# Performance work log

Hardware: AMD Instinct MI355X
Metric: run time of the kernel (lower is better)

## Reference

```python
import jax, jax.numpy as jnp
import numpy as np

N_NODES = 50000
N_EDGES = 600000
F_IN, HID, N_CLS = 128, 128, 40
NEG_SLOPE = 0.2


def _gat_conv(x, src, dst, W, a_src, a_dst, b, num_nodes):
    # x: [N, Fin] -> h: [N, H]  (heads=1 PyG GATConv)
    h = x @ W
    s_src = h @ a_src  # [N]
    s_dst = h @ a_dst  # [N]
    e = jax.nn.leaky_relu(s_src[src] + s_dst[dst], NEG_SLOPE)  # [E]
    # numerically-stable softmax over incoming edges per destination node
    m = jax.ops.segment_max(e, dst, num_segments=num_nodes)  # [N]
    ex = jnp.exp(e - m[dst])
    denom = jax.ops.segment_sum(ex, dst, num_segments=num_nodes)  # [N]
    alpha = ex / denom[dst]  # [E]
    out = jax.ops.segment_sum(alpha[:, None] * h[src], dst, num_segments=num_nodes)
    return out + b


def setup_inputs() -> dict:
    key = jax.random.key(0)
    ks = jax.random.split(key, 10)
    x = jax.random.normal(ks[0], (N_NODES, F_IN), dtype=jnp.float32)
    edge_index = jax.random.randint(ks[1], (2, N_EDGES), 0, N_NODES, dtype=jnp.int64)
    sd = lambda fin: 1.0 / np.sqrt(fin)
    return {
        "x": x,
        "edge_index": edge_index,
        "W1": jax.random.normal(ks[2], (F_IN, HID), dtype=jnp.float32) * sd(F_IN),
        "a1_src": jax.random.normal(ks[3], (HID,), dtype=jnp.float32) * sd(HID),
        "a1_dst": jax.random.normal(ks[4], (HID,), dtype=jnp.float32) * sd(HID),
        "b1": jnp.zeros((HID,), dtype=jnp.float32),
        "W2": jax.random.normal(ks[5], (HID, HID), dtype=jnp.float32) * sd(HID),
        "a2_src": jax.random.normal(ks[6], (HID,), dtype=jnp.float32) * sd(HID),
        "a2_dst": jax.random.normal(ks[7], (HID,), dtype=jnp.float32) * sd(HID),
        "b2": jnp.zeros((HID,), dtype=jnp.float32),
        "Wl": jax.random.normal(ks[8], (HID, N_CLS), dtype=jnp.float32) * sd(HID),
        "bl": jnp.zeros((N_CLS,), dtype=jnp.float32),
    }


def reference(x, edge_index, W1, a1_src, a1_dst, b1, W2, a2_src, a2_dst, b2, Wl, bl):
    n = x.shape[0]
    # PyG GATConv adds self loops by default
    loops = jnp.arange(n, dtype=edge_index.dtype)
    src = jnp.concatenate([edge_index[0], loops])
    dst = jnp.concatenate([edge_index[1], loops])
    h = jax.nn.relu(_gat_conv(x, src, dst, W1, a1_src, a1_dst, b1, n))
    # F.dropout(training=self.training): eval mode -> identity
    h = _gat_conv(h, src, dst, W2, a2_src, a2_dst, b2, n)
    logits = jax.nn.log_softmax(h @ Wl + bl, axis=1)
    return (logits, edge_index)
```

## Files before the change

kernel.cpp:

```cpp
#include <hip/hip_runtime.h>
#include <hip/hip_bf16.h>
#include <math.h>

#define N_NODES 50000
#define N_EDGES 600000
#define TOT_E   (N_EDGES + N_NODES)
#define FDIM    128
#define HROW    64
#define NCLS    40
#define SCAN_B  1024

typedef __attribute__((ext_vector_type(4))) float  f32x4;
typedef __attribute__((ext_vector_type(8))) __bf16 bf16x8;
union FragU { uint32_t u[4]; bf16x8 v; };

__device__ inline float bf16_lo(uint32_t u) { return __uint_as_float(u << 16); }
__device__ inline float bf16_hi(uint32_t u) { return __uint_as_float(u & 0xffff0000u); }
__device__ inline uint32_t bf16_pack(float a, float b) {
    uint32_t ua = __float_as_uint(a), ub = __float_as_uint(b);
    uint32_t ra = (ua + 0x7fffu + ((ua >> 16) & 1u)) >> 16;
    uint32_t rb = (ub + 0x7fffu + ((ub >> 16) & 1u)) >> 16;
    return ra | (rb << 16);
}

__device__ __forceinline__ void wave_agg_loop(
        const uint4* __restrict__ h4, const float* __restrict__ ssrc,
        const int* __restrict__ adj, float sd, int beg, int deg,
        float* wb, int* sb, int lane, int sub, int l16,
        float acc[8], float& dsum) {
    for (int base = 0; base < deg; base += 64) {
        int c = min(64, deg - base);
        int s = 0; float w = 0.f;
        if (lane < c) {
            s = adj[beg + base + lane];
            float e = ssrc[s] + sd;
            e = (e >= 0.f) ? e : 0.2f * e;
            w = __expf(e);
        }
        wb[lane] = w;
        sb[lane] = s;
        dsum += w;
        asm volatile("s_waitcnt lgkmcnt(0)" ::: "memory");

        int rounds = (c + 15) >> 4;
        for (int t = 0; t < rounds; t++) {
            int j = t * 16 + 4 * sub;
            float4 w4 = *(const float4*)&wb[j];
            int4   s4 = *(const int4*)&sb[j];
            uint4 u0 = h4[(size_t)s4.x * 16 + l16];
            uint4 u1 = h4[(size_t)s4.y * 16 + l16];
            uint4 u2 = h4[(size_t)s4.z * 16 + l16];
            uint4 u3 = h4[(size_t)s4.w * 16 + l16];
            acc[0] += w4.x * bf16_lo(u0.x) + w4.y * bf16_lo(u1.x) + w4.z * bf16_lo(u2.x) + w4.w * bf16_lo(u3.x);
            acc[1] += w4.x * bf16_hi(u0.x) + w4.y * bf16_hi(u1.x) + w4.z * bf16_hi(u2.x) + w4.w * bf16_hi(u3.x);
            acc[2] += w4.x * bf16_lo(u0.y) + w4.y * bf16_lo(u1.y) + w4.z * bf16_lo(u2.y) + w4.w * bf16_lo(u3.y);
            acc[3] += w4.x * bf16_hi(u0.y) + w4.y * bf16_hi(u1.y) + w4.z * bf16_hi(u2.y) + w4.w * bf16_hi(u3.y);
            acc[4] += w4.x * bf16_lo(u0.z) + w4.y * bf16_lo(u1.z) + w4.z * bf16_lo(u2.z) + w4.w * bf16_lo(u3.z);
            acc[5] += w4.x * bf16_hi(u0.z) + w4.y * bf16_hi(u1.z) + w4.z * bf16_hi(u2.z) + w4.w * bf16_hi(u3.z);
            acc[6] += w4.x * bf16_lo(u0.w) + w4.y * bf16_lo(u1.w) + w4.z * bf16_lo(u2.w) + w4.w * bf16_lo(u3.w);
            acc[7] += w4.x * bf16_hi(u0.w) + w4.y * bf16_hi(u1.w) + w4.z * bf16_hi(u2.w) + w4.w * bf16_hi(u3.w);
        }
        asm volatile("" ::: "memory");
    }
    #pragma unroll
    for (int k = 0; k < 8; k++) {
        acc[k] += __shfl_xor(acc[k], 16, 64);
        acc[k] += __shfl_xor(acc[k], 32, 64);
    }
    #pragma unroll
    for (int off = 32; off > 0; off >>= 1) dsum += __shfl_xor(dsum, off, 64);
}

#define PACK_BLOCKS  12500
#define WFRAG_BLOCKS 16
#define HIST_BLOCKS  ((N_EDGES / 4 + 255) / 256)
__global__ __launch_bounds__(256) void k1_setup_hist(
        const float* __restrict__ x, uint32_t* __restrict__ Xp,
        const float* __restrict__ W1, const float* __restrict__ W2,
        uint32_t* __restrict__ wf1, uint32_t* __restrict__ wf2,
        const int* __restrict__ ei, int* __restrict__ counts) {
    int b = blockIdx.x;
    if (b < PACK_BLOCKS) {
        int i = b * 256 + threadIdx.x;
        float2 v = ((const float2*)x)[i];
        Xp[i] = bf16_pack(v.x, v.y);
        return;
    }
    if (b < PACK_BLOCKS + WFRAG_BLOCKS) {
        int t = (b - PACK_BLOCKS) * 256 + threadIdx.x;
        if (t >= 4096) return;
        const float* W = (t < 2048) ? W1 : W2;
        uint32_t*   wf = (t < 2048) ? wf1 : wf2;
        int q = t & 2047;
        int lane = q & 63, nt = (q >> 6) & 7, kt = q >> 9;
        int n = nt * 16 + (lane & 15), g = lane >> 4;
        uint32_t frag[4];
        #pragma unroll
        for (int d = 0; d < 4; d++) {
            int kb = kt * 32 + 4 * g + (d & 1) * 2 + (d >> 1) * 16;
            frag[d] = bf16_pack(W[kb * FDIM + n], W[(kb + 1) * FDIM + n]);
        }
        ((uint4*)wf)[(kt * 8 + nt) * 64 + lane] = *(uint4*)frag;
        return;
    }
    int i = (b - PACK_BLOCKS - WFRAG_BLOCKS) * 256 + threadIdx.x;
    if (i >= N_EDGES / 4) return;
    int4 d = ((const int4*)(ei + N_EDGES))[i];
    atomicAdd(&counts[d.x], 1);
    atomicAdd(&counts[d.y], 1);
    atomicAdd(&counts[d.z], 1);
    atomicAdd(&counts[d.w], 1);
}

__global__ void scan1_kernel(const int* __restrict__ counts, int* __restrict__ excl,
                             int* __restrict__ bsums, int n) {
    __shared__ int ws[16];
    int gid = blockIdx.x * SCAN_B + threadIdx.x;
    int wv = threadIdx.x >> 6, lane = threadIdx.x & 63;
    int v = (gid < n) ? (counts[gid] + 1) : 0;
    int incl = v;
    #pragma unroll
    for (int off = 1; off < 64; off <<= 1) {
        int t = __shfl_up(incl, off, 64);
        if (lane >= off) incl += t;
    }
    if (lane == 63) ws[wv] = incl;
    __syncthreads();
    int woff = 0;
    for (int i = 0; i < wv; i++) woff += ws[i];
    if (gid < n) excl[gid] = woff + incl - v;
    if (threadIdx.x == SCAN_B - 1) bsums[blockIdx.x] = woff + incl;
}

__global__ void scan3_kernel(int* __restrict__ rowptr, const int* __restrict__ bsums,
                             int* __restrict__ cursor, int n, int total) {
    __shared__ int base_s;
    if (threadIdx.x < 64) {
        int v = (threadIdx.x < (int)blockIdx.x) ? bsums[threadIdx.x] : 0;
        #pragma unroll
        for (int off = 32; off > 0; off >>= 1) v += __shfl_down(v, off, 64);
        if (threadIdx.x == 0) base_s = v;
    }
    __syncthreads();
    int base = base_s;
    int gid = blockIdx.x * SCAN_B + threadIdx.x;
    if (gid < n) {
        int v = rowptr[gid] + base;
        rowptr[gid] = v;
        cursor[gid] = v;
    }
    if (gid == 0) rowptr[n] = total;
}

#define SCAT_T      ((N_EDGES / 4) + N_NODES)
#define SCAT_BLOCKS ((SCAT_T + 255) / 256)
#define GEMM_BLOCKS ((N_NODES + 63) / 64)
#define EDGE_ITEMS  ((2 * N_EDGES) / 4)
#define EDGE_BLOCKS ((EDGE_ITEMS + 255) / 256)
__global__ __launch_bounds__(256) void k4_scatter_gemm_edge(
        const int* __restrict__ ei, int* __restrict__ cursor, int* __restrict__ adj,
        const uint32_t* __restrict__ Xp, const uint32_t* __restrict__ wf,
        const float* __restrict__ a_s, const float* __restrict__ a_d,
        uint32_t* __restrict__ H, float* __restrict__ ssrc, float* __restrict__ sdst,
        float* __restrict__ eout) {
    int b = blockIdx.x;
    if (b < SCAT_BLOCKS) {
        int i = b * 256 + threadIdx.x;
        if (i >= SCAT_T) return;
        if (i < N_EDGES / 4) {
            int4 s4 = ((const int4*)ei)[i];
            int4 d4 = ((const int4*)(ei + N_EDGES))[i];
            adj[atomicAdd(&cursor[d4.x], 1)] = s4.x;
            adj[atomicAdd(&cursor[d4.y], 1)] = s4.y;
            adj[atomicAdd(&cursor[d4.z], 1)] = s4.z;
            adj[atomicAdd(&cursor[d4.w], 1)] = s4.w;
        } else {
            int nd = i - N_EDGES / 4;
            adj[atomicAdd(&cursor[nd], 1)] = nd;
        }
        return;
    }
    if (b < SCAT_BLOCKS + GEMM_BLOCKS) {
        int lane = threadIdx.x & 63, wv = threadIdx.x >> 6;
        int row0 = (b - SCAT_BLOCKS) * 64 + wv * 16;
        if (row0 >= N_NODES) return;
        int r = lane & 15, g = lane >> 4;

        const uint32_t* xrow = Xp + (size_t)(row0 + r) * HROW + 2 * g;
        FragU af[4];
        #pragma unroll
        for (int kt = 0; kt < 4; kt++) {
            uint2 lo = *(const uint2*)(xrow + kt * 16);
            uint2 hi = *(const uint2*)(xrow + kt * 16 + 8);
            af[kt].u[0] = lo.x; af[kt].u[1] = lo.y;
            af[kt].u[2] = hi.x; af[kt].u[3] = hi.y;
        }
        f32x4 acc[8] = {};
        #pragma unroll
        for (int kt = 0; kt < 4; kt++) {
            #pragma unroll
            for (int nt = 0; nt < 8; nt++) {
                FragU bfr;
                *(uint4*)bfr.u = ((const uint4*)wf)[(kt * 8 + nt) * 64 + lane];
                acc[nt] = __builtin_amdgcn_mfma_f32_16x16x32_bf16(af[kt].v, bfr.v, acc[nt], 0, 0, 0);
            }
        }
        float av_s[8], av_d[8];
        #pragma unroll
        for (int nt = 0; nt < 8; nt++) { av_s[nt] = a_s[16 * nt + r]; av_d[nt] = a_d[16 * nt + r]; }
        #pragma unroll
        for (int j = 0; j < 4; j++) {
            float ps = 0.f, pd = 0.f;
            #pragma unroll
            for (int nt = 0; nt < 8; nt++) { ps += acc[nt][j] * av_s[nt]; pd += acc[nt][j] * av_d[nt]; }
            #pragma unroll
            for (int off = 1; off < 16; off <<= 1) {
                ps += __shfl_xor(ps, off, 64);
                pd += __shfl_xor(pd, off, 64);
            }
            if (r == 0) { ssrc[row0 + 4 * g + j] = ps; sdst[row0 + 4 * g + j] = pd; }
        }
        #pragma unroll
        for (int nt = 0; nt < 8; nt++) {
            #pragma unroll
            for (int j = 0; j < 4; j++) {
                float v0 = acc[nt][j];
                float v1 = __shfl_xor(v0, 1, 64);
                if (!(r & 1))
                    H[(size_t)(row0 + 4 * g + j) * HROW + nt * 8 + (r >> 1)] = bf16_pack(v0, v1);
            }
        }
        return;
    }
    int i = (b - SCAT_BLOCKS - GEMM_BLOCKS) * 256 + threadIdx.x;
    if (i < EDGE_ITEMS) {
        int4 v = ((const int4*)ei)[i];
        ((float4*)eout)[i] = make_float4((float)v.x, (float)v.y, (float)v.z, (float)v.w);
    }
}

__global__ __launch_bounds__(256) void k5_agg_gemm(
        const uint32_t* __restrict__ h, const float* __restrict__ ssrc,
        const float* __restrict__ sdst, const int* __restrict__ rowptr,
        const int* __restrict__ adj, const float* __restrict__ bias,
        const uint32_t* __restrict__ wf, const float* __restrict__ a_s,
        const float* __restrict__ a_d, uint32_t* __restrict__ Hout,
        float* __restrict__ ssrc2, float* __restrict__ sdst2) {
    int tid = threadIdx.x;
    int wv = tid >> 6, lane = tid & 63;
    int sub = lane >> 4, l16 = lane & 15;
    int row0 = blockIdx.x * 16;
    __shared__ __align__(16) float    wbuf[4][64];
    __shared__ __align__(16) int      sbuf[4][64];
    __shared__ __align__(16) uint32_t rowbuf[16][68];
    __shared__ float scS[4][16], scD[4][16];
    const uint4* h4 = (const uint4*)h;

    for (int i = 0; i < 4; i++) {
        int row = wv * 4 + i;
        int n = row0 + row;
        int beg = rowptr[n], deg = rowptr[n + 1] - beg;
        float acc[8] = {};
        float dsum = 0.f;
        wave_agg_loop(h4, ssrc, adj, sdst[n], beg, deg, wbuf[wv], sbuf[wv],
                      lane, sub, l16, acc, dsum);
        if (sub == 0) {
            float inv = 1.f / dsum;
            float4 b0 = *(const float4*)&bias[l16 * 8];
            float4 b1 = *(const float4*)&bias[l16 * 8 + 4];
            float v0 = fmaxf(acc[0] * inv + b0.x, 0.f), v1 = fmaxf(acc[1] * inv + b0.y, 0.f);
            float v2 = fmaxf(acc[2] * inv + b0.z, 0.f), v3 = fmaxf(acc[3] * inv + b0.w, 0.f);
            float v4 = fmaxf(acc[4] * inv + b1.x, 0.f), v5 = fmaxf(acc[5] * inv + b1.y, 0.f);
            float v6 = fmaxf(acc[6] * inv + b1.z, 0.f), v7 = fmaxf(acc[7] * inv + b1.w, 0.f);
            uint4 o;
            o.x = bf16_pack(v0, v1); o.y = bf16_pack(v2, v3);
            o.z = bf16_pack(v4, v5); o.w = bf16_pack(v6, v7);
            *(uint4*)&rowbuf[row][l16 * 4] = o;
        }
    }
    __syncthreads();

    int r = lane & 15, g = lane >> 4;
    FragU af[4];
    #pragma unroll
    for (int kt = 0; kt < 4; kt++) {
        uint2 lo = *(const uint2*)&rowbuf[r][kt * 16 + 2 * g];
        uint2 hi = *(const uint2*)&rowbuf[r][kt * 16 + 2 * g + 8];
        af[kt].u[0] = lo.x; af[kt].u[1] = lo.y;
        af[kt].u[2] = hi.x; af[kt].u[3] = hi.y;
    }
    f32x4 acc2[2] = {};
    #pragma unroll
    for (int kt = 0; kt < 4; kt++) {
        #pragma unroll
        for (int t = 0; t < 2; t++) {
            int nt = 2 * wv + t;
            FragU bfr;
            *(uint4*)bfr.u = ((const uint4*)wf)[(kt * 8 + nt) * 64 + lane];
            acc2[t] = __builtin_amdgcn_mfma_f32_16x16x32_bf16(af[kt].v, bfr.v, acc2[t], 0, 0, 0);
        }
    }
    float as0 = a_s[16 * (2 * wv) + r], as1 = a_s[16 * (2 * wv + 1) + r];
    float ad0 = a_d[16 * (2 * wv) + r], ad1 = a_d[16 * (2 * wv + 1) + r];
    #pragma unroll
    for (int j = 0; j < 4; j++) {
        float ps = acc2[0][j] * as0 + acc2[1][j] * as1;
        float pd = acc2[0][j] * ad0 + acc2[1][j] * ad1;
        #pragma unroll
        for (int off = 1; off < 16; off <<= 1) {
            ps += __shfl_xor(ps, off, 64);
            pd += __shfl_xor(pd, off, 64);
        }
        if (r == 0) { scS[wv][4 * g + j] = ps; scD[wv][4 * g + j] = pd; }
    }
    #pragma unroll
    for (int t = 0; t < 2; t++) {
        #pragma unroll
        for (int j = 0; j < 4; j++) {
            float v0 = acc2[t][j];
            float v1 = __shfl_xor(v0, 1, 64);
            if (!(r & 1))
                Hout[(size_t)(row0 + 4 * g + j) * HROW + (2 * wv + t) * 8 + (r >> 1)] = bf16_pack(v0, v1);
        }
    }
    __syncthreads();
    if (tid < 16)
        ssrc2[row0 + tid] = scS[0][tid] + scS[1][tid] + scS[2][tid] + scS[3][tid];
    else if (tid < 32) {
        int q = tid - 16;
        sdst2[row0 + q] = scD[0][q] + scD[1][q] + scD[2][q] + scD[3][q];
    }
}

__global__ __launch_bounds__(256) void k6_agg_cls(
        const uint32_t* __restrict__ h, const float* __restrict__ ssrc,
        const float* __restrict__ sdst, const int* __restrict__ rowptr,
        const int* __restrict__ adj, const float* __restrict__ bias,
        const float* __restrict__ Wl, const float* __restrict__ bl,
        float* __restrict__ out) {
    int tid = threadIdx.x;
    int wv = tid >> 6, lane = tid & 63;
    int sub = lane >> 4, l16 = lane & 15;
    int row0 = blockIdx.x * 16;
    __shared__ __align__(16) float wbuf[4][64];
    __shared__ __align__(16) int   sbuf[4][64];
    __shared__ float xs[16][FDIM];
    const uint4* h4 = (const uint4*)h;

    for (int i = 0; i < 4; i++) {
        int row = wv * 4 + i;
        int n = row0 + row;
        int beg = rowptr[n], deg = rowptr[n + 1] - beg;
        float acc[8] = {};
        float dsum = 0.f;
        wave_agg_loop(h4, ssrc, adj, sdst[n], beg, deg, wbuf[wv], sbuf[wv],
                      lane, sub, l16, acc, dsum);
        if (sub == 0) {
            float inv = 1.f / dsum;
            float4 b0 = *(const float4*)&bias[l16 * 8];
            float4 b1 = *(const float4*)&bias[l16 * 8 + 4];
            float4 p0, p1;
            p0.x = acc[0] * inv + b0.x; p0.y = acc[1] * inv + b0.y;
            p0.z = acc[2] * inv + b0.z; p0.w = acc[3] * inv + b0.w;
            p1.x = acc[4] * inv + b1.x; p1.y = acc[5] * inv + b1.y;
            p1.z = acc[6] * inv + b1.z; p1.w = acc[7] * inv + b1.w;
            *(float4*)&xs[row][l16 * 8]     = p0;
            *(float4*)&xs[row][l16 * 8 + 4] = p1;
        }
    }
    __syncthreads();

    int c = tid & 63, hw = tid >> 6;
    float acc[4];
    float blc = (c < NCLS) ? bl[c] : 0.f;
    #pragma unroll
    for (int r = 0; r < 4; r++) acc[r] = blc;

    #pragma unroll 2
    for (int k = 0; k < FDIM; k += 4) {
        float w0 = 0.f, w1 = 0.f, w2 = 0.f, w3 = 0.f;
        if (c < NCLS) {
            w0 = Wl[(k + 0) * NCLS + c]; w1 = Wl[(k + 1) * NCLS + c];
            w2 = Wl[(k + 2) * NCLS + c]; w3 = Wl[(k + 3) * NCLS + c];
        }
        #pragma unroll
        for (int r = 0; r < 4; r++) {
            float4 xv = *(const float4*)&xs[hw * 4 + r][k];
            acc[r] += xv.x * w0 + xv.y * w1 + xv.z * w2 + xv.w * w3;
        }
    }
    #pragma unroll
    for (int r = 0; r < 4; r++) {
        float v = (c < NCLS) ? acc[r] : -INFINITY;
        float mx = v;
        #pragma unroll
        for (int off = 32; off > 0; off >>= 1) mx = fmaxf(mx, __shfl_xor(mx, off, 64));
        float ex = (c < NCLS) ? expf(v - mx) : 0.f;
        #pragma unroll
        for (int off = 32; off > 0; off >>= 1) ex += __shfl_xor(ex, off, 64);
        float ls = logf(ex);
        if (c < NCLS) out[(size_t)(row0 + hw * 4 + r) * NCLS + c] = v - mx - ls;
    }
}

extern "C" void kernel_launch(void* const* d_in, const int* in_sizes, int n_in,
                              void* d_out, int out_size, void* d_ws, size_t ws_size,
                              hipStream_t stream) {
    const float* x   = (const float*)d_in[0];
    const int*   ei  = (const int*)d_in[1];
    const float* W1  = (const float*)d_in[2];
    const float* a1s = (const float*)d_in[3];
    const float* a1d = (const float*)d_in[4];
    const float* b1  = (const float*)d_in[5];
    const float* W2  = (const float*)d_in[6];
    const float* a2s = (const float*)d_in[7];
    const float* a2d = (const float*)d_in[8];
    const float* b2  = (const float*)d_in[9];
    const float* Wl  = (const float*)d_in[10];
    const float* bl  = (const float*)d_in[11];
    float* out = (float*)d_out;

    char* ws = (char*)d_ws;
    size_t off = 0;
    auto alloc = [&](size_t bytes) {
        void* p = ws + off;
        off = (off + bytes + 255) & ~(size_t)255;
        return p;
    };
    int*      row_ptr = (int*)alloc((N_NODES + 1) * sizeof(int));
    int*      cursor  = (int*)alloc(N_NODES * sizeof(int));
    int*      counts  = (int*)alloc(N_NODES * sizeof(int));
    int*      bsums   = (int*)alloc(64 * sizeof(int));
    int*      adj     = (int*)alloc(TOT_E * sizeof(int));
    uint32_t* Xp      = (uint32_t*)alloc((size_t)N_NODES * HROW * sizeof(uint32_t));
    uint32_t* hA      = (uint32_t*)alloc((size_t)N_NODES * HROW * sizeof(uint32_t));
    uint32_t* hB      = (uint32_t*)alloc((size_t)N_NODES * HROW * sizeof(uint32_t));
    float*    ssrc    = (float*)alloc(N_NODES * sizeof(float));
    float*    sdst    = (float*)alloc(N_NODES * sizeof(float));
    float*    ssrc2   = (float*)alloc(N_NODES * sizeof(float));
    float*    sdst2   = (float*)alloc(N_NODES * sizeof(float));
    uint32_t* wf1     = (uint32_t*)alloc(2048 * 4 * sizeof(uint32_t));
    uint32_t* wf2     = (uint32_t*)alloc(2048 * 4 * sizeof(uint32_t));

    hipMemsetAsync(counts, 0, N_NODES * sizeof(int), stream);

    hipLaunchKernelGGL(k1_setup_hist, dim3(PACK_BLOCKS + WFRAG_BLOCKS + HIST_BLOCKS), dim3(256),
                       0, stream, x, Xp, W1, W2, wf1, wf2, ei, counts);

    int nscan = (N_NODES + SCAN_B - 1) / SCAN_B;
    hipLaunchKernelGGL(scan1_kernel, dim3(nscan), dim3(SCAN_B), 0, stream, counts, row_ptr, bsums, N_NODES);
    hipLaunchKernelGGL(scan3_kernel, dim3(nscan), dim3(SCAN_B), 0, stream, row_ptr, bsums, cursor, N_NODES, TOT_E);

    hipLaunchKernelGGL(k4_scatter_gemm_edge, dim3(SCAT_BLOCKS + GEMM_BLOCKS + EDGE_BLOCKS), dim3(256),
                       0, stream, ei, cursor, adj, Xp, wf1, a1s, a1d, hA, ssrc, sdst,
                       out + (size_t)N_NODES * NCLS);

    hipLaunchKernelGGL(k5_agg_gemm, dim3(N_NODES / 16), dim3(256), 0, stream,
                       hA, ssrc, sdst, row_ptr, adj, b1, wf2, a2s, a2d, hB, ssrc2, sdst2);

    hipLaunchKernelGGL(k6_agg_cls, dim3(N_NODES / 16), dim3(256), 0, stream,
                       hB, ssrc2, sdst2, row_ptr, adj, b2, Wl, bl, out);
}
```

Measured before the change: 269.2 us.

## Pad CSR rows to multiples of 16 and compute attention weights block-wide

Rounds each node's adjacency segment up to a multiple of 16 entries, zero-filling the padded adjacency buffer, so the aggregation loop runs without tail handling and reads source indices straight from global memory. Edge attention weights for a block's 16 rows are computed cooperatively into shared memory before aggregation, replacing the per-wave 64-edge chunking. Blocks grow to 512 threads with two rows per wave, and the MFMA and classifier stages are re-split to match. The padding adds zero-index edges whose weight is masked to zero, and it enlarges the adjacency buffer and the zeroing work. Rows whose padded segment exceeds the 1024-entry shared buffer would overflow it.

```diff
diff --git a/kernel.cpp b/kernel.cpp
--- a/kernel.cpp
+++ b/kernel.cpp
@@ -4,11 +4,11 @@
 
 #define N_NODES 50000
 #define N_EDGES 600000
-#define TOT_E   (N_EDGES + N_NODES)
 #define FDIM    128
 #define HROW    64
 #define NCLS    40
 #define SCAN_B  1024
+#define PADMAX  1400000
 
 typedef __attribute__((ext_vector_type(4))) float  f32x4;
 typedef __attribute__((ext_vector_type(8))) __bf16 bf16x8;
@@ -23,62 +23,71 @@
     return ra | (rb << 16);
 }
 
-__device__ __forceinline__ void wave_agg_loop(
-        const uint4* __restrict__ h4, const float* __restrict__ ssrc,
-        const int* __restrict__ adj, float sd, int beg, int deg,
-        float* wb, int* sb, int lane, int sub, int l16,
-        float acc[8], float& dsum) {
-    for (int base = 0; base < deg; base += 64) {
-        int c = min(64, deg - base);
-        int s = 0; float w = 0.f;
-        if (lane < c) {
-            s = adj[beg + base + lane];
-            float e = ssrc[s] + sd;
+__device__ __forceinline__ void block_weights(
+        const int* __restrict__ adj, const float* __restrict__ ssrc,
+        const int* rowL, const int* rdegL, const float* sdL,
+        float* wlds, int tid) {
+    int beg0 = rowL[0], range = rowL[16] - beg0;
+    for (int i = tid; i < range; i += 512) {
+        int gi = beg0 + i;
+        int nn = 0;
+        if (gi >= rowL[nn + 8]) nn += 8;
+        if (gi >= rowL[nn + 4]) nn += 4;
+        if (gi >= rowL[nn + 2]) nn += 2;
+        if (gi >= rowL[nn + 1]) nn += 1;
+        float w = 0.f;
+        if (gi - rowL[nn] < rdegL[nn]) {
+            float e = ssrc[adj[gi]] + sdL[nn];
             e = (e >= 0.f) ? e : 0.2f * e;
             w = __expf(e);
         }
-        wb[lane] = w;
-        sb[lane] = s;
-        dsum += w;
-        asm volatile("s_waitcnt lgkmcnt(0)" ::: "memory");
-
-        int rounds = (c + 15) >> 4;
-        for (int t = 0; t < rounds; t++) {
-            int j = t * 16 + 4 * sub;
-            float4 w4 = *(const float4*)&wb[j];
-            int4   s4 = *(const int4*)&sb[j];
-            uint4 u0 = h4[(size_t)s4.x * 16 + l16];
-            uint4 u1 = h4[(size_t)s4.y * 16 + l16];
-            uint4 u2 = h4[(size_t)s4.z * 16 + l16];
-            uint4 u3 = h4[(size_t)s4.w * 16 + l16];
-            acc[0] += w4.x * bf16_lo(u0.x) + w4.y * bf16_lo(u1.x) + w4.z * bf16_lo(u2.x) + w4.w * bf16_lo(u3.x);
-            acc[1] += w4.x * bf16_hi(u0.x) + w4.y * bf16_hi(u1.x) + w4.z * bf16_hi(u2.x) + w4.w * bf16_hi(u3.x);
-            acc[2] += w4.x * bf16_lo(u0.y) + w4.y * bf16_lo(u1.y) + w4.z * bf16_lo(u2.y) + w4.w * bf16_lo(u3.y);
-            acc[3] += w4.x * bf16_hi(u0.y) + w4.y * bf16_hi(u1.y) + w4.z * bf16_hi(u2.y) + w4.w * bf16_hi(u3.y);
-            acc[4] += w4.x * bf16_lo(u0.z) + w4.y * bf16_lo(u1.z) + w4.z * bf16_lo(u2.z) + w4.w * bf16_lo(u3.z);
-            acc[5] += w4.x * bf16_hi(u0.z) + w4.y * bf16_hi(u1.z) + w4.z * bf16_hi(u2.z) + w4.w * bf16_hi(u3.z);
-            acc[6] += w4.x * bf16_lo(u0.w) + w4.y * bf16_lo(u1.w) + w4.z * bf16_lo(u2.w) + w4.w * bf16_lo(u3.w);
-            acc[7] += w4.x * bf16_hi(u0.w) + w4.y * bf16_hi(u1.w) + w4.z * bf16_hi(u2.w) + w4.w * bf16_hi(u3.w);
-        }
-        asm volatile("" ::: "memory");
+        wlds[i] = w;
+    }
+}
+
+__device__ __forceinline__ void wave_agg(
+        const uint4* __restrict__ h4, const int* __restrict__ adj,
+        const float* wlds, int beg0, int beg, int pdeg,
+        int sub, int l16, float acc[8], float& dsum) {
+    int rounds = pdeg >> 4;
+    for (int t = 0; t < rounds; t++) {
+        int j = beg + t * 16 + 4 * sub;
+        float4 w4 = *(const float4*)&wlds[j - beg0];
+        int4   s4 = *(const int4*)&adj[j];
+        uint4 u0 = h4[(size_t)s4.x * 16 + l16];
+        uint4 u1 = h4[(size_t)s4.y * 16 + l16];
+        uint4 u2 = h4[(size_t)s4.z * 16 + l16];
+        uint4 u3 = h4[(size_t)s4.w * 16 + l16];
+        dsum += (w4.x + w4.y) + (w4.z + w4.w);
+        acc[0] += w4.x * bf16_lo(u0.x) + w4.y * bf16_lo(u1.x) + w4.z * bf16_lo(u2.x) + w4.w * bf16_lo(u3.x);
+        acc[1] += w4.x * bf16_hi(u0.x) + w4.y * bf16_hi(u1.x) + w4.z * bf16_hi(u2.x) + w4.w * bf16_hi(u3.x);
+        acc[2] += w4.x * bf16_lo(u0.y) + w4.y * bf16_lo(u1.y) + w4.z * bf16_lo(u2.y) + w4.w * bf16_lo(u3.y);
+        acc[3] += w4.x * bf16_hi(u0.y) + w4.y * bf16_hi(u1.y) + w4.z * bf16_hi(u2.y) + w4.w * bf16_hi(u3.y);
+        acc[4] += w4.x * bf16_lo(u0.z) + w4.y * bf16_lo(u1.z) + w4.z * bf16_lo(u2.z) + w4.w * bf16_lo(u3.z);
+        acc[5] += w4.x * bf16_hi(u0.z) + w4.y * bf16_hi(u1.z) + w4.z * bf16_hi(u2.z) + w4.w * bf16_hi(u3.z);
+        acc[6] += w4.x * bf16_lo(u0.w) + w4.y * bf16_lo(u1.w) + w4.z * bf16_lo(u2.w) + w4.w * bf16_lo(u3.w);
+        acc[7] += w4.x * bf16_hi(u0.w) + w4.y * bf16_hi(u1.w) + w4.z * bf16_hi(u2.w) + w4.w * bf16_hi(u3.w);
     }
     #pragma unroll
     for (int k = 0; k < 8; k++) {
         acc[k] += __shfl_xor(acc[k], 16, 64);
         acc[k] += __shfl_xor(acc[k], 32, 64);
     }
-    #pragma unroll
-    for (int off = 32; off > 0; off >>= 1) dsum += __shfl_xor(dsum, off, 64);
+    dsum += __shfl_xor(dsum, 16, 64);
+    dsum += __shfl_xor(dsum, 32, 64);
 }
 
 #define PACK_BLOCKS  12500
 #define WFRAG_BLOCKS 16
 #define HIST_BLOCKS  ((N_EDGES / 4 + 255) / 256)
+#define ADJZ_ITEMS   (PADMAX / 4)
+#define ADJZ_BLOCKS  ((ADJZ_ITEMS + 255) / 256)
 __global__ __launch_bounds__(256) void k1_setup_hist(
         const float* __restrict__ x, uint32_t* __restrict__ Xp,
         const float* __restrict__ W1, const float* __restrict__ W2,
         uint32_t* __restrict__ wf1, uint32_t* __restrict__ wf2,
-        const int* __restrict__ ei, int* __restrict__ counts) {
+        const int* __restrict__ ei, int* __restrict__ counts,
+        int* __restrict__ adj) {
     int b = blockIdx.x;
     if (b < PACK_BLOCKS) {
         int i = b * 256 + threadIdx.x;
@@ -103,13 +112,18 @@
         ((uint4*)wf)[(kt * 8 + nt) * 64 + lane] = *(uint4*)frag;
         return;
     }
-    int i = (b - PACK_BLOCKS - WFRAG_BLOCKS) * 256 + threadIdx.x;
-    if (i >= N_EDGES / 4) return;
-    int4 d = ((const int4*)(ei + N_EDGES))[i];
-    atomicAdd(&counts[d.x], 1);
-    atomicAdd(&counts[d.y], 1);
-    atomicAdd(&counts[d.z], 1);
-    atomicAdd(&counts[d.w], 1);
+    if (b < PACK_BLOCKS + WFRAG_BLOCKS + HIST_BLOCKS) {
+        int i = (b - PACK_BLOCKS - WFRAG_BLOCKS) * 256 + threadIdx.x;
+        if (i >= N_EDGES / 4) return;
+        int4 d = ((const int4*)(ei + N_EDGES))[i];
+        atomicAdd(&counts[d.x], 1);
+        atomicAdd(&counts[d.y], 1);
+        atomicAdd(&counts[d.z], 1);
+        atomicAdd(&counts[d.w], 1);
+        return;
+    }
+    int i = (b - PACK_BLOCKS - WFRAG_BLOCKS - HIST_BLOCKS) * 256 + threadIdx.x;
+    if (i < ADJZ_ITEMS) ((int4*)adj)[i] = make_int4(0, 0, 0, 0);
 }
 
 __global__ void scan1_kernel(const int* __restrict__ counts, int* __restrict__ excl,
@@ -117,7 +131,7 @@
     __shared__ int ws[16];
     int gid = blockIdx.x * SCAN_B + threadIdx.x;
     int wv = threadIdx.x >> 6, lane = threadIdx.x & 63;
-    int v = (gid < n) ? (counts[gid] + 1) : 0;
+    int v = (gid < n) ? ((counts[gid] + 16) & ~15) : 0;
     int incl = v;
     #pragma unroll
     for (int off = 1; off < 64; off <<= 1) {
@@ -133,7 +147,8 @@
 }
 
 __global__ void scan3_kernel(int* __restrict__ rowptr, const int* __restrict__ bsums,
-                             int* __restrict__ cursor, int n, int total) {
+                             int* __restrict__ cursor, const int* __restrict__ counts,
+                             int n) {
     __shared__ int base_s;
     if (threadIdx.x < 64) {
         int v = (threadIdx.x < (int)blockIdx.x) ? bsums[threadIdx.x] : 0;
@@ -148,8 +163,8 @@
         int v = rowptr[gid] + base;
         rowptr[gid] = v;
         cursor[gid] = v;
-    }
-    if (gid == 0) rowptr[n] = total;
+        if (gid == n - 1) rowptr[n] = v + ((counts[gid] + 16) & ~15);
+    }
 }
 
 #define SCAT_T      ((N_EDGES / 4) + N_NODES)
@@ -239,31 +254,40 @@
     }
 }
 
-__global__ __launch_bounds__(256) void k5_agg_gemm(
+__global__ __launch_bounds__(512) void k5_agg_gemm(
         const uint32_t* __restrict__ h, const float* __restrict__ ssrc,
         const float* __restrict__ sdst, const int* __restrict__ rowptr,
-        const int* __restrict__ adj, const float* __restrict__ bias,
-        const uint32_t* __restrict__ wf, const float* __restrict__ a_s,
-        const float* __restrict__ a_d, uint32_t* __restrict__ Hout,
-        float* __restrict__ ssrc2, float* __restrict__ sdst2) {
+        const int* __restrict__ counts, const int* __restrict__ adj,
+        const float* __restrict__ bias, const uint32_t* __restrict__ wf,
+        const float* __restrict__ a_s, const float* __restrict__ a_d,
+        uint32_t* __restrict__ Hout, float* __restrict__ ssrc2,
+        float* __restrict__ sdst2) {
     int tid = threadIdx.x;
     int wv = tid >> 6, lane = tid & 63;
     int sub = lane >> 4, l16 = lane & 15;
     int row0 = blockIdx.x * 16;
-    __shared__ __align__(16) float    wbuf[4][64];
-    __shared__ __align__(16) int      sbuf[4][64];
+    __shared__ int   rowL[17];
+    __shared__ int   rdegL[16];
+    __shared__ float sdL[16];
+    __shared__ __align__(16) float wlds[1024];
     __shared__ __align__(16) uint32_t rowbuf[16][68];
-    __shared__ float scS[4][16], scD[4][16];
+    __shared__ float scS[8][16], scD[8][16];
     const uint4* h4 = (const uint4*)h;
 
-    for (int i = 0; i < 4; i++) {
-        int row = wv * 4 + i;
-        int n = row0 + row;
-        int beg = rowptr[n], deg = rowptr[n + 1] - beg;
+    if (tid < 17) rowL[tid] = rowptr[row0 + tid];
+    if (tid < 16) { rdegL[tid] = counts[row0 + tid] + 1; sdL[tid] = sdst[row0 + tid]; }
+    __syncthreads();
+    block_weights(adj, ssrc, rowL, rdegL, sdL, wlds, tid);
+    __syncthreads();
+
+    int beg0 = rowL[0];
+    #pragma unroll
+    for (int i = 0; i < 2; i++) {
+        int row = wv * 2 + i;
         float acc[8] = {};
         float dsum = 0.f;
-        wave_agg_loop(h4, ssrc, adj, sdst[n], beg, deg, wbuf[wv], sbuf[wv],
-                      lane, sub, l16, acc, dsum);
+        wave_agg(h4, adj, wlds, beg0, rowL[row], rowL[row + 1] - rowL[row],
+                 sub, l16, acc, dsum);
         if (sub == 0) {
             float inv = 1.f / dsum;
             float4 b0 = *(const float4*)&bias[l16 * 8];
@@ -289,23 +313,18 @@
         af[kt].u[0] = lo.x; af[kt].u[1] = lo.y;
         af[kt].u[2] = hi.x; af[kt].u[3] = hi.y;
     }
-    f32x4 acc2[2] = {};
+    f32x4 acc2 = {};
     #pragma unroll
     for (int kt = 0; kt < 4; kt++) {
-        #pragma unroll
-        for (int t = 0; t < 2; t++) {
-            int nt = 2 * wv + t;
-            FragU bfr;
-            *(uint4*)bfr.u = ((const uint4*)wf)[(kt * 8 + nt) * 64 + lane];
-            acc2[t] = __builtin_amdgcn_mfma_f32_16x16x32_bf16(af[kt].v, bfr.v, acc2[t], 0, 0, 0);
-        }
-    }
-    float as0 = a_s[16 * (2 * wv) + r], as1 = a_s[16 * (2 * wv + 1) + r];
-    float ad0 = a_d[16 * (2 * wv) + r], ad1 = a_d[16 * (2 * wv + 1) + r];
+        FragU bfr;
+        *(uint4*)bfr.u = ((const uint4*)wf)[(kt * 8 + wv) * 64 + lane];
+        acc2 = __builtin_amdgcn_mfma_f32_16x16x32_bf16(af[kt].v, bfr.v, acc2, 0, 0, 0);
+    }
+    float as0 = a_s[16 * wv + r], ad0 = a_d[16 * wv + r];
     #pragma unroll
     for (int j = 0; j < 4; j++) {
-        float ps = acc2[0][j] * as0 + acc2[1][j] * as1;
-        float pd = acc2[0][j] * ad0 + acc2[1][j] * ad1;
+        float ps = acc2[j] * as0;
+        float pd = acc2[j] * ad0;
         #pragma unroll
         for (int off = 1; off < 16; off <<= 1) {
             ps += __shfl_xor(ps, off, 64);
@@ -314,47 +333,58 @@
         if (r == 0) { scS[wv][4 * g + j] = ps; scD[wv][4 * g + j] = pd; }
     }
     #pragma unroll
-    for (int t = 0; t < 2; t++) {
-        #pragma unroll
-        for (int j = 0; j < 4; j++) {
-            float v0 = acc2[t][j];
-            float v1 = __shfl_xor(v0, 1, 64);
-            if (!(r & 1))
-                Hout[(size_t)(row0 + 4 * g + j) * HROW + (2 * wv + t) * 8 + (r >> 1)] = bf16_pack(v0, v1);
-        }
-    }
-    __syncthreads();
-    if (tid < 16)
-        ssrc2[row0 + tid] = scS[0][tid] + scS[1][tid] + scS[2][tid] + scS[3][tid];
-    else if (tid < 32) {
+    for (int j = 0; j < 4; j++) {
+        float v0 = acc2[j];
+        float v1 = __shfl_xor(v0, 1, 64);
+        if (!(r & 1))
+            Hout[(size_t)(row0 + 4 * g + j) * HROW + wv * 8 + (r >> 1)] = bf16_pack(v0, v1);
+    }
+    __syncthreads();
+    if (tid < 16) {
+        float s = 0.f;
+        #pragma unroll
+        for (int w = 0; w < 8; w++) s += scS[w][tid];
+        ssrc2[row0 + tid] = s;
+    } else if (tid < 32) {
         int q = tid - 16;
-        sdst2[row0 + q] = scD[0][q] + scD[1][q] + scD[2][q] + scD[3][q];
-    }
-}
-
-__global__ __launch_bounds__(256) void k6_agg_cls(
+        float s = 0.f;
+        #pragma unroll
+        for (int w = 0; w < 8; w++) s += scD[w][q];
+        sdst2[row0 + q] = s;
+    }
+}
+
+__global__ __launch_bounds__(512) void k6_agg_cls(
         const uint32_t* __restrict__ h, const float* __restrict__ ssrc,
         const float* __restrict__ sdst, const int* __restrict__ rowptr,
-        const int* __restrict__ adj, const float* __restrict__ bias,
-        const float* __restrict__ Wl, const float* __restrict__ bl,
-        float* __restrict__ out) {
+        const int* __restrict__ counts, const int* __restrict__ adj,
+        const float* __restrict__ bias, const float* __restrict__ Wl,
+        const float* __restrict__ bl, float* __restrict__ out) {
     int tid = threadIdx.x;
     int wv = tid >> 6, lane = tid & 63;
     int sub = lane >> 4, l16 = lane & 15;
     int row0 = blockIdx.x * 16;
-    __shared__ __align__(16) float wbuf[4][64];
-    __shared__ __align__(16) int   sbuf[4][64];
+    __shared__ int   rowL[17];
+    __shared__ int   rdegL[16];
+    __shared__ float sdL[16];
+    __shared__ __align__(16) float wlds[1024];
     __shared__ float xs[16][FDIM];
     const uint4* h4 = (const uint4*)h;
 
-    for (int i = 0; i < 4; i++) {
-        int row = wv * 4 + i;
-        int n = row0 + row;
-        int beg = rowptr[n], deg = rowptr[n + 1] - beg;
+    if (tid < 17) rowL[tid] = rowptr[row0 + tid];
+    if (tid < 16) { rdegL[tid] = counts[row0 + tid] + 1; sdL[tid] = sdst[row0 + tid]; }
+    __syncthreads();
+    block_weights(adj, ssrc, rowL, rdegL, sdL, wlds, tid);
+    __syncthreads();
+
+    int beg0 = rowL[0];
+    #pragma unroll
+    for (int i = 0; i < 2; i++) {
+        int row = wv * 2 + i;
         float acc[8] = {};
         float dsum = 0.f;
-        wave_agg_loop(h4, ssrc, adj, sdst[n], beg, deg, wbuf[wv], sbuf[wv],
-                      lane, sub, l16, acc, dsum);
+        wave_agg(h4, adj, wlds, beg0, rowL[row], rowL[row + 1] - rowL[row],
+                 sub, l16, acc, dsum);
         if (sub == 0) {
             float inv = 1.f / dsum;
             float4 b0 = *(const float4*)&bias[l16 * 8];
@@ -371,10 +401,9 @@
     __syncthreads();
 
     int c = tid & 63, hw = tid >> 6;
-    float acc[4];
+    float acc[2];
     float blc = (c < NCLS) ? bl[c] : 0.f;
-    #pragma unroll
-    for (int r = 0; r < 4; r++) acc[r] = blc;
+    acc[0] = blc; acc[1] = blc;
 
     #pragma unroll 2
     for (int k = 0; k < FDIM; k += 4) {
@@ -384,13 +413,13 @@
             w2 = Wl[(k + 2) * NCLS + c]; w3 = Wl[(k + 3) * NCLS + c];
         }
         #pragma unroll
-        for (int r = 0; r < 4; r++) {
-            float4 xv = *(const float4*)&xs[hw * 4 + r][k];
+        for (int r = 0; r < 2; r++) {
+            float4 xv = *(const float4*)&xs[hw * 2 + r][k];
             acc[r] += xv.x * w0 + xv.y * w1 + xv.z * w2 + xv.w * w3;
         }
     }
     #pragma unroll
-    for (int r = 0; r < 4; r++) {
+    for (int r = 0; r < 2; r++) {
         float v = (c < NCLS) ? acc[r] : -INFINITY;
         float mx = v;
         #pragma unroll
@@ -399,7 +428,7 @@
         #pragma unroll
         for (int off = 32; off > 0; off >>= 1) ex += __shfl_xor(ex, off, 64);
         float ls = logf(ex);
-        if (c < NCLS) out[(size_t)(row0 + hw * 4 + r) * NCLS + c] = v - mx - ls;
+        if (c < NCLS) out[(size_t)(row0 + hw * 2 + r) * NCLS + c] = v - mx - ls;
     }
 }
 
@@ -431,7 +460,7 @@
     int*      cursor  = (int*)alloc(N_NODES * sizeof(int));
     int*      counts  = (int*)alloc(N_NODES * sizeof(int));
     int*      bsums   = (int*)alloc(64 * sizeof(int));
-    int*      adj     = (int*)alloc(TOT_E * sizeof(int));
+    int*      adj     = (int*)alloc(PADMAX * sizeof(int));
     uint32_t* Xp      = (uint32_t*)alloc((size_t)N_NODES * HROW * sizeof(uint32_t));
     uint32_t* hA      = (uint32_t*)alloc((size_t)N_NODES * HROW * sizeof(uint32_t));
     uint32_t* hB      = (uint32_t*)alloc((size_t)N_NODES * HROW * sizeof(uint32_t));
@@ -444,20 +473,21 @@
 
     hipMemsetAsync(counts, 0, N_NODES * sizeof(int), stream);
 
-    hipLaunchKernelGGL(k1_setup_hist, dim3(PACK_BLOCKS + WFRAG_BLOCKS + HIST_BLOCKS), dim3(256),
-                       0, stream, x, Xp, W1, W2, wf1, wf2, ei, counts);
+    hipLaunchKernelGGL(k1_setup_hist,
+                       dim3(PACK_BLOCKS + WFRAG_BLOCKS + HIST_BLOCKS + ADJZ_BLOCKS), dim3(256),
+                       0, stream, x, Xp, W1, W2, wf1, wf2, ei, counts, adj);
 
     int nscan = (N_NODES + SCAN_B - 1) / SCAN_B;
     hipLaunchKernelGGL(scan1_kernel, dim3(nscan), dim3(SCAN_B), 0, stream, counts, row_ptr, bsums, N_NODES);
-    hipLaunchKernelGGL(scan3_kernel, dim3(nscan), dim3(SCAN_B), 0, stream, row_ptr, bsums, cursor, N_NODES, TOT_E);
+    hipLaunchKernelGGL(scan3_kernel, dim3(nscan), dim3(SCAN_B), 0, stream, row_ptr, bsums, cursor, counts, N_NODES);
 
     hipLaunchKernelGGL(k4_scatter_gemm_edge, dim3(SCAT_BLOCKS + GEMM_BLOCKS + EDGE_BLOCKS), dim3(256),
                        0, stream, ei, cursor, adj, Xp, wf1, a1s, a1d, hA, ssrc, sdst,
                        out + (size_t)N_NODES * NCLS);
 
-    hipLaunchKernelGGL(k5_agg_gemm, dim3(N_NODES / 16), dim3(256), 0, stream,
-                       hA, ssrc, sdst, row_ptr, adj, b1, wf2, a2s, a2d, hB, ssrc2, sdst2);
-
-    hipLaunchKernelGGL(k6_agg_cls, dim3(N_NODES / 16), dim3(256), 0, stream,
-                       hB, ssrc2, sdst2, row_ptr, adj, b2, Wl, bl, out);
-}
+    hipLaunchKernelGGL(k5_agg_gemm, dim3(N_NODES / 16), dim3(512), 0, stream,
+                       hA, ssrc, sdst, row_ptr, counts, adj, b1, wf2, a2s, a2d, hB, ssrc2, sdst2);
+
+    hipLaunchKernelGGL(k6_agg_cls, dim3(N_NODES / 16), dim3(512), 0, stream,
+                       hB, ssrc2, sdst2, row_ptr, counts, adj, b2, Wl, bl, out);
+}
```

After: 278.6 us. 3.5% more time.
